# Kernel tuning notes

Hardware: AMD Instinct MI355X
Metric: run time of the kernel (lower is better)

Reference implementation:

```python
import jax, jax.numpy as jnp
import numpy as np

DIM = 180
WS = 16        # window_size
OWS = 24       # overlap_win_size = int(16*0.5)+16
HEADS = 6
HD = DIM // HEADS
MLP_HID = DIM * 2
TABLE = (WS + OWS - 1) ** 2  # 1521
H = W = 256
B = 1


def layernorm(x, g, b, eps=1e-5):
    mu = x.mean(-1, keepdims=True)
    d = x - mu
    var = (d * d).mean(-1, keepdims=True)
    return g * d / jnp.sqrt(var + eps) + b


def setup_inputs() -> dict:
    key = jax.random.key(0)
    ks = jax.random.split(key, 12)
    std = 0.02
    inp = {
        'x': jax.random.normal(ks[0], (B, H * W, DIM), jnp.float32),
        'rpi': jax.random.randint(ks[1], (WS * WS, OWS * OWS), 0, TABLE, jnp.int32),
        'h': H,
        'w': W,
        'norm1_g': jnp.ones((DIM,), jnp.float32),
        'norm1_b': jnp.zeros((DIM,), jnp.float32),
        'q_w': jax.random.normal(ks[2], (DIM, DIM), jnp.float32) * std,
        'q_b': jnp.zeros((DIM,), jnp.float32),
        'kv_w': jax.random.normal(ks[3], (DIM, 2 * DIM), jnp.float32) * std,
        'kv_b': jnp.zeros((2 * DIM,), jnp.float32),
        'rpb_table': jax.random.normal(ks[4], (TABLE, HEADS), jnp.float32) * std,
        'proj_w': jax.random.normal(ks[5], (DIM, DIM), jnp.float32) * std,
        'proj_b': jnp.zeros((DIM,), jnp.float32),
        'norm2_g': jnp.ones((DIM,), jnp.float32),
        'norm2_b': jnp.zeros((DIM,), jnp.float32),
        'mlp_w1': jax.random.normal(ks[6], (DIM, MLP_HID), jnp.float32) * std,
        'mlp_b1': jnp.zeros((MLP_HID,), jnp.float32),
        'mlp_w2': jax.random.normal(ks[7], (MLP_HID, DIM), jnp.float32) * std,
        'mlp_b2': jnp.zeros((DIM,), jnp.float32),
    }
    return inp


def reference(x, rpi, h, w, norm1_g, norm1_b, q_w, q_b, kv_w, kv_b,
              rpb_table, proj_w, proj_b, norm2_g, norm2_b,
              mlp_w1, mlp_b1, mlp_w2, mlp_b2):
    b, L, c = x.shape
    ws, ows, heads = WS, OWS, HEADS
    d = c // heads
    scale = d ** -0.5
    pad = (ows - ws) // 2  # 4
    nh, nw = h // ws, w // ws
    nq, n = ws * ws, ows * ows
    b_ = b * nh * nw

    shortcut = x
    xn = layernorm(x, norm1_g, norm1_b)
    x_img = xn.reshape(b, h, w, c)

    q = x_img @ q_w + q_b                    # [b,h,w,c]
    kv = x_img @ kv_w + kv_b                 # [b,h,w,2c] (k | v)

    # window_partition for q -> [b_, nq, c]
    qw = q.reshape(b, nh, ws, nw, ws, c).transpose(0, 1, 3, 2, 4, 5)
    qw = qw.reshape(b_, nq, c)

    # nn.Unfold(kernel=ows, stride=ws, padding=pad) on kv -> overlapping windows
    kvp = jnp.pad(kv, ((0, 0), (pad, pad), (pad, pad), (0, 0)))
    rows = (jnp.arange(nh) * ws)[:, None] + jnp.arange(ows)   # [nh, ows]
    cols = (jnp.arange(nw) * ws)[:, None] + jnp.arange(ows)   # [nw, ows]
    t = kvp[:, rows]                         # [b, nh, ows, W+2p, 2c]
    t = t[:, :, :, cols]                     # [b, nh, ows, nw, ows, 2c]
    t = t.transpose(0, 1, 3, 2, 4, 5).reshape(b_, n, 2 * c)
    k_win, v_win = t[..., :c], t[..., c:]

    qh = qw.reshape(b_, nq, heads, d).transpose(0, 2, 1, 3) * scale
    kh = k_win.reshape(b_, n, heads, d).transpose(0, 2, 1, 3)
    vh = v_win.reshape(b_, n, heads, d).transpose(0, 2, 1, 3)

    attn = jnp.einsum('bhqd,bhkd->bhqk', qh, kh)              # [b_,heads,nq,n]
    bias = rpb_table[rpi.reshape(-1)].reshape(nq, n, heads).transpose(2, 0, 1)
    attn = jax.nn.softmax(attn + bias[None], axis=-1)
    out = jnp.einsum('bhqk,bhkd->bhqd', attn, vh)
    out = out.transpose(0, 2, 1, 3).reshape(b_, nq, c)

    # window_reverse -> [b, h*w, c]
    xo = out.reshape(b, nh, nw, ws, ws, c).transpose(0, 1, 3, 2, 4, 5)
    xo = xo.reshape(b, h * w, c)

    xo = xo @ proj_w + proj_b + shortcut
    xn2 = layernorm(xo, norm2_g, norm2_b)
    mlp = jax.nn.gelu(xn2 @ mlp_w1 + mlp_b1, approximate=False) @ mlp_w2 + mlp_b2
    return xo + mlp
```

## Files before the change

kernel.cpp:

```cpp
#include <hip/hip_runtime.h>
#include <hip/hip_bf16.h>
#include <stdint.h>

#define DIM 180
#define WS 16
#define OWS 24
#define HEADS 6
#define HD 30
#define MLP_HID 360
#define HH 256
#define WW 256
#define L (HH * WW)
#define NWIN 256
#define NQ 256
#define NK 576

#define KP1 192
#define KP2 384
#define NQKV 576

#define QSCALE 0.2633988734672831f
#define LOG2E 1.4426950408889634f

typedef float f4v __attribute__((ext_vector_type(4)));
typedef short s8v __attribute__((ext_vector_type(8)));
typedef short s4v __attribute__((ext_vector_type(4)));

static __device__ __forceinline__ short f2bf(float x) {
    union { __hip_bfloat16 h; short s; } u;
    u.h = __float2bfloat16(x);
    return u.s;
}
static __device__ __forceinline__ uint32_t pack_bf2(float lo, float hi) {
    union { __hip_bfloat162 h; uint32_t u; } u;
    u.h.x = __float2bfloat16(lo);
    u.h.y = __float2bfloat16(hi);
    return u.u;
}

typedef __attribute__((address_space(1))) const unsigned int ga_u32;
typedef __attribute__((address_space(3))) unsigned int la_u32;
static __device__ __forceinline__ void gld16(const void* g, void* l) {
    __builtin_amdgcn_global_load_lds((ga_u32*)g, (la_u32*)l, 16, 0, 0);
}

__global__ __launch_bounds__(64) void ln_kernel(const float* __restrict__ x,
                                                const float* __restrict__ g,
                                                const float* __restrict__ b,
                                                __hip_bfloat16* __restrict__ out) {
    int row = blockIdx.x;
    int t = threadIdx.x;
    const float* xr = x + (size_t)row * DIM;
    float v0 = xr[t];
    float v1 = xr[t + 64];
    float v2 = (t < DIM - 128) ? xr[t + 128] : 0.f;
    float s = v0 + v1 + v2;
    #pragma unroll
    for (int o = 32; o > 0; o >>= 1) s += __shfl_down(s, o);
    s = __shfl(s, 0);
    float mu = s * (1.f / DIM);
    float d0 = v0 - mu, d1 = v1 - mu;
    float d2 = (t < DIM - 128) ? (v2 - mu) : 0.f;
    float vs = d0 * d0 + d1 * d1 + d2 * d2;
    #pragma unroll
    for (int o = 32; o > 0; o >>= 1) vs += __shfl_down(vs, o);
    vs = __shfl(vs, 0);
    float rstd = rsqrtf(vs * (1.f / DIM) + 1e-5f);
    __hip_bfloat16* orow = out + (size_t)row * KP1;
    orow[t]      = __float2bfloat16(g[t] * d0 * rstd + b[t]);
    orow[t + 64] = __float2bfloat16(g[t + 64] * d1 * rstd + b[t + 64]);
    if (t < DIM - 128)
        orow[t + 128] = __float2bfloat16(g[t + 128] * d2 * rstd + b[t + 128]);
    if (t < KP1 - DIM) orow[DIM + t] = __float2bfloat16(0.f);
}

__global__ __launch_bounds__(256) void bias_kernel(const int* __restrict__ rpi,
                                                   const float* __restrict__ rpb,
                                                   float* __restrict__ biasC) {
    int idx = blockIdx.x * 256 + threadIdx.x;
    int j = idx & 15;
    int q = (idx >> 4) & 255;
    int r = idx >> 12;
    int kc = r % 36;
    int head = r / 36;
    int k = kc * 16 + j;
    int t = rpi[q * NK + k];
    biasC[idx] = rpb[t * HEADS + head] * LOG2E;
}

__global__ __launch_bounds__(256) void wconv_kernel(
        const float* __restrict__ qw, const float* __restrict__ kvw,
        const float* __restrict__ pw, const float* __restrict__ w1,
        const float* __restrict__ w2, short* __restrict__ wt) {
    int idx = blockIdx.x * 256 + threadIdx.x;
    float v = 0.f;
    if (idx < 110592) {
        int n = idx / KP1, k = idx - n * KP1;
        if (k < DIM) {
            if (n < DIM) v = qw[k * DIM + n] * QSCALE;
            else if (n < 540) v = kvw[k * (2 * DIM) + (n - DIM)];
        }
    } else if (idx < 147456) {
        int r = idx - 110592;
        int n = r / KP1, k = r - n * KP1;
        if (k < DIM && n < DIM) v = pw[k * DIM + n];
    } else if (idx < 221184) {
        int r = idx - 147456;
        int n = r / KP1, k = r - n * KP1;
        if (k < DIM && n < MLP_HID) v = w1[k * MLP_HID + n];
    } else {
        int r = idx - 221184;
        int n = r / KP2, k = r - n * KP2;
        if (k < MLP_HID && n < DIM) v = w2[k * DIM + n];
    }
    wt[idx] = f2bf(v);
}

__global__ __launch_bounds__(256) void bconv_kernel(
        const float* __restrict__ qb, const float* __restrict__ kvb,
        const float* __restrict__ pb, const float* __restrict__ b1,
        const float* __restrict__ b2, float* __restrict__ bv) {
    int idx = blockIdx.x * 256 + threadIdx.x;
    if (idx >= 1344) return;
    float v = 0.f;
    if (idx < 576) {
        if (idx < DIM) v = qb[idx] * QSCALE;
        else if (idx < 540) v = kvb[idx - DIM];
    } else if (idx < 768) {
        int n = idx - 576; if (n < DIM) v = pb[n];
    } else if (idx < 1152) {
        int n = idx - 768; if (n < MLP_HID) v = b1[n];
    } else {
        int n = idx - 1152; if (n < DIM) v = b2[n];
    }
    bv[idx] = v;
}

__global__ __launch_bounds__(256) void mgemm(
        const short* __restrict__ A, const short* __restrict__ Wt,
        const float* __restrict__ bias,
        float* __restrict__ outf, short* __restrict__ outb,
        int lda, int ldo, int nK, int mode) {
    __shared__ short As[2][128 * 32];
    __shared__ short Wsm[2][64 * 32];
    int tid = threadIdx.x;
    int lane = tid & 63, wave = tid >> 6;
    int q15 = lane & 15, quad = lane >> 4;
    int n0 = blockIdx.x * 64;
    int m0 = blockIdx.y * 128;

    auto stage = [&](int buf, int k0) {
        int lr = lane >> 2, c = lane & 3;
        const short* Ab = A + (size_t)m0 * lda + k0;
        #pragma unroll
        for (int i = 0; i < 2; i++) {
            int r = i * 64 + wave * 16 + lr;
            gld16(Ab + (size_t)r * lda + ((c ^ (r & 3)) * 8),
                  &As[buf][(i * 64 + wave * 16) * 32]);
        }
        const short* Wb = Wt + (size_t)n0 * lda + k0;
        {
            int r = wave * 16 + lr;
            gld16(Wb + (size_t)r * lda + ((c ^ (r & 3)) * 8),
                  &Wsm[buf][(wave * 16) * 32]);
        }
    };

    f4v acc[2][4];
    #pragma unroll
    for (int a = 0; a < 2; a++)
        #pragma unroll
        for (int b = 0; b < 4; b++) acc[a][b] = (f4v){0.f, 0.f, 0.f, 0.f};

    stage(0, 0);
    __syncthreads();
    for (int ch = 0; ch < nK; ch++) {
        int buf = ch & 1;
        if (ch + 1 < nK) stage(buf ^ 1, (ch + 1) * 32);
        s8v af[2], wf[4];
        #pragma unroll
        for (int mt = 0; mt < 2; mt++) {
            int r = wave * 32 + mt * 16 + q15;
            af[mt] = *(const s8v*)&As[buf][r * 32 + ((quad ^ (r & 3)) * 8)];
        }
        #pragma unroll
        for (int nt = 0; nt < 4; nt++) {
            int r = nt * 16 + q15;
            wf[nt] = *(const s8v*)&Wsm[buf][r * 32 + ((quad ^ (r & 3)) * 8)];
        }
        #pragma unroll
        for (int mt = 0; mt < 2; mt++)
            #pragma unroll
            for (int nt = 0; nt < 4; nt++)
                acc[mt][nt] = __builtin_amdgcn_mfma_f32_16x16x32_bf16(
                    af[mt], wf[nt], acc[mt][nt], 0, 0, 0);
        __syncthreads();
    }

    #pragma unroll
    for (int mt = 0; mt < 2; mt++) {
        int mb = m0 + wave * 32 + mt * 16 + quad * 4;
        #pragma unroll
        for (int nt = 0; nt < 4; nt++) {
            int n = n0 + nt * 16 + q15;
            float bv = bias[n];
            f4v a = acc[mt][nt];
            #pragma unroll
            for (int r = 0; r < 4; r++) {
                int m = mb + r;
                float v = a[r] + bv;
                if (mode == 0) {
                    outb[(size_t)m * ldo + n] = f2bf(v);
                } else if (mode == 1) {
                    float ge = 0.5f * v * (1.f + erff(v * 0.70710678118654752f));
                    outb[(size_t)m * ldo + n] = f2bf(ge);
                } else {
                    if (n < DIM) outf[(size_t)m * DIM + n] += v;
                }
            }
        }
    }
}

__global__ __launch_bounds__(256) void projln(
        const short* __restrict__ A, const short* __restrict__ Wt,
        const float* __restrict__ bias, const float* __restrict__ resid,
        const float* __restrict__ g2, const float* __restrict__ b2,
        float* __restrict__ outf, short* __restrict__ outb) {
    __shared__ short As[2][64 * 32];
    __shared__ short Wsm[2][192 * 32];
    int tid = threadIdx.x;
    int lane = tid & 63, wave = tid >> 6;
    int q15 = lane & 15, quad = lane >> 4;
    int m0 = blockIdx.x * 64;

    auto stage = [&](int buf, int k0) {
        int lr = lane >> 2, c = lane & 3;
        const short* Ab = A + (size_t)m0 * KP1 + k0;
        {
            int r = wave * 16 + lr;
            gld16(Ab + (size_t)r * KP1 + ((c ^ (r & 3)) * 8),
                  &As[buf][(wave * 16) * 32]);
        }
        #pragma unroll
        for (int i = 0; i < 3; i++) {
            int r = i * 64 + wave * 16 + lr;
            gld16(Wt + (size_t)r * KP1 + k0 + ((c ^ (r & 3)) * 8),
                  &Wsm[buf][(i * 64 + wave * 16) * 32]);
        }
    };

    f4v acc[12];
    #pragma unroll
    for (int b = 0; b < 12; b++) acc[b] = (f4v){0.f, 0.f, 0.f, 0.f};

    stage(0, 0);
    __syncthreads();
    for (int ch = 0; ch < KP1 / 32; ch++) {
        int buf = ch & 1;
        if (ch + 1 < KP1 / 32) stage(buf ^ 1, (ch + 1) * 32);
        int ra = wave * 16 + q15;
        s8v af = *(const s8v*)&As[buf][ra * 32 + ((quad ^ (ra & 3)) * 8)];
        #pragma unroll
        for (int nt = 0; nt < 12; nt++) {
            int r = nt * 16 + q15;
            s8v wf = *(const s8v*)&Wsm[buf][r * 32 + ((quad ^ (r & 3)) * 8)];
            acc[nt] = __builtin_amdgcn_mfma_f32_16x16x32_bf16(af, wf, acc[nt], 0, 0, 0);
        }
        __syncthreads();
    }

    float gv[12], bv[12], biasv[12];
    #pragma unroll
    for (int nt = 0; nt < 12; nt++) {
        int n = nt * 16 + q15;
        biasv[nt] = bias[n];
        gv[nt] = (n < DIM) ? g2[n] : 0.f;
        bv[nt] = (n < DIM) ? b2[n] : 0.f;
    }
    int mb = m0 + wave * 16 + quad * 4;
    #pragma unroll
    for (int r = 0; r < 4; r++) {
        int m = mb + r;
        float v[12];
        float s = 0.f, ss = 0.f;
        #pragma unroll
        for (int nt = 0; nt < 12; nt++) {
            int n = nt * 16 + q15;
            float x = acc[nt][r] + biasv[nt];
            if (n < DIM) x += resid[(size_t)m * DIM + n];
            else x = 0.f;
            v[nt] = x;
            s += x;
            ss += x * x;
        }
        #pragma unroll
        for (int o = 8; o > 0; o >>= 1) {
            s += __shfl_xor(s, o);
            ss += __shfl_xor(ss, o);
        }
        float mu = s * (1.f / DIM);
        float var = ss * (1.f / DIM) - mu * mu;
        float rstd = rsqrtf(var + 1e-5f);
        #pragma unroll
        for (int nt = 0; nt < 12; nt++) {
            int n = nt * 16 + q15;
            if (n < DIM) outf[(size_t)m * DIM + n] = v[nt];
            outb[(size_t)m * KP1 + n] = f2bf(gv[nt] * (v[nt] - mu) * rstd + bv[nt]);
        }
    }
}

#define CHUNK 32
#define NCHUNK (NK / CHUNK)

__global__ __launch_bounds__(256) void attn_kernel(
        const __hip_bfloat16* __restrict__ qkvb,
        const float* __restrict__ biasC, __hip_bfloat16* __restrict__ aout) {
    __shared__ __align__(16) short Ks[2][CHUNK][32];
    __shared__ __align__(16) short Vt[2][32][40];
    __shared__ __align__(16) short Ps[256][40];

    int tid = threadIdx.x;
    int lane = tid & 63;
    int wave = tid >> 6;
    int q15 = lane & 15;
    int quad = lane >> 4;
    int head = blockIdx.x % HEADS;
    int win = blockIdx.x / HEADS;
    int bh = win >> 4, bw = win & 15;

    const uint32_t* kvd = (const uint32_t*)qkvb;

    s8v qf[4];
    #pragma unroll
    for (int qt = 0; qt < 4; qt++) {
        int q = wave * 64 + qt * 16 + q15;
        int qy = q >> 4, qx = q & 15;
        size_t pos = (size_t)(bh * WS + qy) * WW + (bw * WS + qx);
        const uint32_t* qp = kvd + pos * 288 + head * 15 + quad * 4;
        uint32_t w0 = qp[0], w1 = qp[1], w2 = qp[2], w3 = qp[3];
        union { uint32_t u[4]; s8v v; } cv;
        cv.u[0] = w0; cv.u[1] = w1; cv.u[2] = w2; cv.u[3] = w3;
        qf[qt] = cv.v;
    }
    if (head == 0) {
        int qy = tid >> 4, qx = tid & 15;
        size_t pos = (size_t)(bh * WS + qy) * WW + (bw * WS + qx);
        uint2 z = make_uint2(0u, 0u);
        uint2* oz = (uint2*)(aout + pos * KP1 + DIM);
        oz[0] = z; oz[1] = z; oz[2] = z;
    }

    uint32_t ka, kb, va, vb;
    int keyK = tid >> 3, pK = tid & 7;
    int keyV = tid & 31, pp = tid >> 5;

    auto rowbase = [&](int jk) -> const uint32_t* {
        int oy = jk / OWS, ox = jk - oy * OWS;
        int y = bh * WS - 4 + oy, x = bw * WS - 4 + ox;
        if ((unsigned)y < HH && (unsigned)x < WW)
            return kvd + ((size_t)y * WW + x) * 288;
        return nullptr;
    };
    auto loadKV = [&](int c0) {
        ka = kb = va = vb = 0u;
        const uint32_t* rk = rowbase(c0 + keyK);
        if (rk) {
            const uint32_t* kp = rk + 90 + head * 15 + pK * 2;
            ka = kp[0];
            if (pK < 7) kb = kp[1];
        }
        const uint32_t* rv = rowbase(c0 + keyV);
        if (rv) {
            const uint32_t* vp = rv + 180 + head * 15 + pp * 2;
            va = vp[0];
            if (pp < 7) vb = vp[1];
        }
    };
    auto writeKV = [&](int bufi) {
        *(uint2*)&Ks[bufi][keyK][pK * 4] = make_uint2(ka, kb);
        int d0 = pp * 4;
        Vt[bufi][d0][keyV]     = (short)(va & 0xffff);
        Vt[bufi][d0 + 1][keyV] = (short)(va >> 16);
        if (pp < 7) {
            Vt[bufi][d0 + 2][keyV] = (short)(vb & 0xffff);
            Vt[bufi][d0 + 3][keyV] = (short)(vb >> 16);
        } else {
            Vt[bufi][30][keyV] = (short)0x3F80;
            Vt[bufi][31][keyV] = 0;
        }
    };

    loadKV(0);
    writeKV(0);
    __syncthreads();

    f4v oacc[2][4];
    #pragma unroll
    for (int a = 0; a < 2; a++)
        #pragma unroll
        for (int b = 0; b < 4; b++) oacc[a][b] = (f4v){0.f, 0.f, 0.f, 0.f};

    const float* bC = biasC + (size_t)head * (36 * 256 * 16);

    for (int ch = 0; ch < NCHUNK; ch++) {
        int buf = ch & 1;
        if (ch + 1 < NCHUNK) loadKV((ch + 1) * CHUNK);

        s8v kf[2];
        #pragma unroll
        for (int kt = 0; kt < 2; kt++)
            kf[kt] = *(const s8v*)&Ks[buf][kt * 16 + q15][quad * 8];
        #pragma unroll
        for (int qt = 0; qt < 4; qt++) {
            int q = wave * 64 + qt * 16 + q15;
            #pragma unroll
            for (int kt = 0; kt < 2; kt++) {
                int kc = ch * 2 + kt;
                f4v c = *(const f4v*)(bC + ((size_t)kc * 256 + q) * 16 + quad * 4);
                c = __builtin_amdgcn_mfma_f32_16x16x32_bf16(kf[kt], qf[qt], c, 0, 0, 0);
                s4v pk;
                #pragma unroll
                for (int r = 0; r < 4; r++)
                    pk[r] = f2bf(__builtin_amdgcn_exp2f(c[r]));
                *(s4v*)&Ps[q][kt * 16 + quad * 4] = pk;
            }
        }

        s8v va0 = *(const s8v*)&Vt[buf][q15][quad * 8];
        s8v va1 = *(const s8v*)&Vt[buf][16 + q15][quad * 8];
        #pragma unroll
        for (int nt = 0; nt < 4; nt++) {
            s8v pb = *(const s8v*)&Ps[wave * 64 + nt * 16 + q15][quad * 8];
            oacc[0][nt] = __builtin_amdgcn_mfma_f32_16x16x32_bf16(va0, pb, oacc[0][nt], 0, 0, 0);
            oacc[1][nt] = __builtin_amdgcn_mfma_f32_16x16x32_bf16(va1, pb, oacc[1][nt], 0, 0, 0);
        }

        if (ch + 1 < NCHUNK) writeKV(buf ^ 1);
        __syncthreads();
    }

    #pragma unroll
    for (int nt = 0; nt < 4; nt++) {
        float l = __shfl(oacc[1][nt][2], 48 | q15);
        float rl = 1.0f / l;
        int q = wave * 64 + nt * 16 + q15;
        int qy = q >> 4, qx = q & 15;
        size_t pos = (size_t)(bh * WS + qy) * WW + (bw * WS + qx);
        uint32_t* od = (uint32_t*)(aout + pos * KP1 + head * HD);
        int dh = quad * 2;
        f4v o0 = oacc[0][nt], o1 = oacc[1][nt];
        od[dh]     = pack_bf2(o0[0] * rl, o0[1] * rl);
        od[dh + 1] = pack_bf2(o0[2] * rl, o0[3] * rl);
        od[8 + dh] = pack_bf2(o1[0] * rl, o1[1] * rl);
        if (quad < 3)
            od[8 + dh + 1] = pack_bf2(o1[2] * rl, o1[3] * rl);
    }
}

extern "C" void kernel_launch(void* const* d_in, const int* in_sizes, int n_in,
                              void* d_out, int out_size, void* d_ws, size_t ws_size,
                              hipStream_t stream) {
    const float* x      = (const float*)d_in[0];
    const int*   rpi    = (const int*)d_in[1];
    const float* n1g    = (const float*)d_in[4];
    const float* n1b    = (const float*)d_in[5];
    const float* q_w    = (const float*)d_in[6];
    const float* q_b    = (const float*)d_in[7];
    const float* kv_w   = (const float*)d_in[8];
    const float* kv_b   = (const float*)d_in[9];
    const float* rpb    = (const float*)d_in[10];
    const float* proj_w = (const float*)d_in[11];
    const float* proj_b = (const float*)d_in[12];
    const float* n2g    = (const float*)d_in[13];
    const float* n2b    = (const float*)d_in[14];
    const float* w1     = (const float*)d_in[15];
    const float* b1     = (const float*)d_in[16];
    const float* w2     = (const float*)d_in[17];
    const float* b2     = (const float*)d_in[18];
    float* out = (float*)d_out;

    char* ws = (char*)d_ws;
    short* qkvb  = (short*)(ws);
    short* xn    = (short*)(ws + 75497472ull);
    float* biasC = (float*)(ws + 100663296ull);
    short* wt    = (short*)(ws + 104202240ull);
    short* wt_qkv  = wt;
    short* wt_proj = wt + 110592;
    short* wt_1    = wt + 147456;
    short* wt_2    = wt + 221184;
    float* bvec  = (float*)(ws + 104202240ull + 589824ull);
    float* b_qkv  = bvec;
    float* b_proj = bvec + 576;
    float* b_1    = bvec + 768;
    float* b_2    = bvec + 1152;
    short* ao  = xn;
    short* xn2 = qkvb;
    short* h1  = qkvb + 12582912;

    bias_kernel<<<884736 / 256, 256, 0, stream>>>(rpi, rpb, biasC);
    wconv_kernel<<<294912 / 256, 256, 0, stream>>>(q_w, kv_w, proj_w, w1, w2, wt);
    bconv_kernel<<<6, 256, 0, stream>>>(q_b, kv_b, proj_b, b1, b2, bvec);
    ln_kernel<<<L, 64, 0, stream>>>(x, n1g, n1b, (__hip_bfloat16*)xn);
    mgemm<<<dim3(NQKV / 64, L / 128), 256, 0, stream>>>(
        xn, wt_qkv, b_qkv, nullptr, qkvb, KP1, NQKV, KP1 / 32, 0);
    attn_kernel<<<NWIN * HEADS, 256, 0, stream>>>(
        (const __hip_bfloat16*)qkvb, biasC, (__hip_bfloat16*)ao);
    projln<<<L / 64, 256, 0, stream>>>(
        ao, wt_proj, b_proj, x, n2g, n2b, out, xn2);
    mgemm<<<dim3(KP2 / 64, L / 128), 256, 0, stream>>>(
        xn2, wt_1, b_1, nullptr, h1, KP1, KP2, KP1 / 32, 1);
    mgemm<<<dim3(KP1 / 64, L / 128), 256, 0, stream>>>(
        h1, wt_2, b_2, out, nullptr, KP2, 0, KP2 / 32, 3);
}
```

Before: 422.3 us.

## Keep softmax probabilities in registers by permuting key order across MFMAs

The attention kernel no longer stages exp'd scores through a shared-memory P buffer. It permutes which key rows feed each QK MFMA, and reorders the precomputed bias layout to match, so that the QK output fragment lines up directly with the B-operand layout of the PV MFMA. The probabilities are packed in registers and fed straight into the PV MFMA. This removes LDS writes and reads plus their bank traffic and frees LDS for occupancy, but it depends on the key permutation being consistent between bias, K rows and V rows.

After: 435.8 us. +3.2%, slower.

```diff
diff --git a/kernel.cpp b/kernel.cpp
--- a/kernel.cpp
+++ b/kernel.cpp
@@ -83,7 +83,7 @@
     int r = idx >> 12;
     int kc = r % 36;
     int head = r / 36;
-    int k = kc * 16 + j;
+    int k = (kc >> 1) * 32 + ((j >> 2) << 3) + ((kc & 1) << 2) + (j & 3);
     int t = rpi[q * NK + k];
     biasC[idx] = rpb[t * HEADS + head] * LOG2E;
 }
@@ -319,7 +319,6 @@
         const float* __restrict__ biasC, __hip_bfloat16* __restrict__ aout) {
     __shared__ __align__(16) short Ks[2][CHUNK][32];
     __shared__ __align__(16) short Vt[2][32][40];
-    __shared__ __align__(16) short Ps[256][40];
 
     int tid = threadIdx.x;
     int lane = tid & 63;
@@ -403,38 +402,32 @@
         for (int b = 0; b < 4; b++) oacc[a][b] = (f4v){0.f, 0.f, 0.f, 0.f};
 
     const float* bC = biasC + (size_t)head * (36 * 256 * 16);
+    int pr = ((q15 & 12) << 1) | (q15 & 3);
 
     for (int ch = 0; ch < NCHUNK; ch++) {
         int buf = ch & 1;
         if (ch + 1 < NCHUNK) loadKV((ch + 1) * CHUNK);
 
-        s8v kf[2];
-        #pragma unroll
-        for (int kt = 0; kt < 2; kt++)
-            kf[kt] = *(const s8v*)&Ks[buf][kt * 16 + q15][quad * 8];
+        s8v kf0 = *(const s8v*)&Ks[buf][pr][quad * 8];
+        s8v kf1 = *(const s8v*)&Ks[buf][pr + 4][quad * 8];
+        s8v va0 = *(const s8v*)&Vt[buf][q15][quad * 8];
+        s8v va1 = *(const s8v*)&Vt[buf][16 + q15][quad * 8];
+
+        const float* bc0 = bC + ((size_t)(ch * 2) * 256) * 16 + quad * 4;
         #pragma unroll
         for (int qt = 0; qt < 4; qt++) {
             int q = wave * 64 + qt * 16 + q15;
-            #pragma unroll
-            for (int kt = 0; kt < 2; kt++) {
-                int kc = ch * 2 + kt;
-                f4v c = *(const f4v*)(bC + ((size_t)kc * 256 + q) * 16 + quad * 4);
-                c = __builtin_amdgcn_mfma_f32_16x16x32_bf16(kf[kt], qf[qt], c, 0, 0, 0);
-                s4v pk;
-                #pragma unroll
-                for (int r = 0; r < 4; r++)
-                    pk[r] = f2bf(__builtin_amdgcn_exp2f(c[r]));
-                *(s4v*)&Ps[q][kt * 16 + quad * 4] = pk;
-            }
-        }
-
-        s8v va0 = *(const s8v*)&Vt[buf][q15][quad * 8];
-        s8v va1 = *(const s8v*)&Vt[buf][16 + q15][quad * 8];
-        #pragma unroll
-        for (int nt = 0; nt < 4; nt++) {
-            s8v pb = *(const s8v*)&Ps[wave * 64 + nt * 16 + q15][quad * 8];
-            oacc[0][nt] = __builtin_amdgcn_mfma_f32_16x16x32_bf16(va0, pb, oacc[0][nt], 0, 0, 0);
-            oacc[1][nt] = __builtin_amdgcn_mfma_f32_16x16x32_bf16(va1, pb, oacc[1][nt], 0, 0, 0);
+            f4v c0 = *(const f4v*)(bc0 + (size_t)q * 16);
+            f4v c1 = *(const f4v*)(bc0 + 256 * 16 + (size_t)q * 16);
+            c0 = __builtin_amdgcn_mfma_f32_16x16x32_bf16(kf0, qf[qt], c0, 0, 0, 0);
+            c1 = __builtin_amdgcn_mfma_f32_16x16x32_bf16(kf1, qf[qt], c1, 0, 0, 0);
+            union { uint32_t u[4]; s8v v; } pbv;
+            pbv.u[0] = pack_bf2(__builtin_amdgcn_exp2f(c0[0]), __builtin_amdgcn_exp2f(c0[1]));
+            pbv.u[1] = pack_bf2(__builtin_amdgcn_exp2f(c0[2]), __builtin_amdgcn_exp2f(c0[3]));
+            pbv.u[2] = pack_bf2(__builtin_amdgcn_exp2f(c1[0]), __builtin_amdgcn_exp2f(c1[1]));
+            pbv.u[3] = pack_bf2(__builtin_amdgcn_exp2f(c1[2]), __builtin_amdgcn_exp2f(c1[3]));
+            oacc[0][qt] = __builtin_amdgcn_mfma_f32_16x16x32_bf16(va0, pbv.v, oacc[0][qt], 0, 0, 0);
+            oacc[1][qt] = __builtin_amdgcn_mfma_f32_16x16x32_bf16(va1, pbv.v, oacc[1][qt], 0, 0, 0);
         }
 
         if (ch + 1 < NCHUNK) writeKV(buf ^ 1);
```

## Keep attention probabilities in registers and deepen KV/bias prefetch pipeline

Applied to the files above, without the earlier changes.

Removes the shared-memory P staging buffer by permuting K rows so the QK^T MFMA output layout directly matches the B-operand layout of the PV MFMA, packing exp2 results into registers. The bias table is reordered to match this permuted key order. KV global loads are now prefetched two chunks ahead using alternating register sets, and bias for the next chunk is loaded early into the accumulator registers. This cuts LDS traffic and hides global latency, at the cost of higher register pressure.

After: 418.6 us. Within noise of the previous version (-0.9%).

```diff
diff --git a/kernel.cpp b/kernel.cpp
--- a/kernel.cpp
+++ b/kernel.cpp
@@ -83,7 +83,7 @@
     int r = idx >> 12;
     int kc = r % 36;
     int head = r / 36;
-    int k = kc * 16 + j;
+    int k = (kc >> 1) * 32 + ((j >> 2) << 3) + ((kc & 1) << 2) + (j & 3);
     int t = rpi[q * NK + k];
     biasC[idx] = rpb[t * HEADS + head] * LOG2E;
 }
@@ -319,7 +319,6 @@
         const float* __restrict__ biasC, __hip_bfloat16* __restrict__ aout) {
     __shared__ __align__(16) short Ks[2][CHUNK][32];
     __shared__ __align__(16) short Vt[2][32][40];
-    __shared__ __align__(16) short Ps[256][40];
 
     int tid = threadIdx.x;
     int lane = tid & 63;
@@ -352,7 +351,6 @@
         oz[0] = z; oz[1] = z; oz[2] = z;
     }
 
-    uint32_t ka, kb, va, vb;
     int keyK = tid >> 3, pK = tid & 7;
     int keyV = tid & 31, pp = tid >> 5;
 
@@ -363,7 +361,7 @@
             return kvd + ((size_t)y * WW + x) * 288;
         return nullptr;
     };
-    auto loadKV = [&](int c0) {
+    auto loadKV = [&](int c0, uint32_t& ka, uint32_t& kb, uint32_t& va, uint32_t& vb) {
         ka = kb = va = vb = 0u;
         const uint32_t* rk = rowbase(c0 + keyK);
         if (rk) {
@@ -378,7 +376,7 @@
             if (pp < 7) vb = vp[1];
         }
     };
-    auto writeKV = [&](int bufi) {
+    auto writeKV = [&](int bufi, uint32_t ka, uint32_t kb, uint32_t va, uint32_t vb) {
         *(uint2*)&Ks[bufi][keyK][pK * 4] = make_uint2(ka, kb);
         int d0 = pp * 4;
         Vt[bufi][d0][keyV]     = (short)(va & 0xffff);
@@ -392,8 +390,24 @@
         }
     };
 
-    loadKV(0);
-    writeKV(0);
+    const float* bC  = biasC + (size_t)head * (36 * 256 * 16);
+    const float* bCl = bC + ((size_t)(wave * 64 + q15)) * 16 + quad * 4;
+    f4v cb[2][4];
+    auto loadBias = [&](int ch) {
+        #pragma unroll
+        for (int kt = 0; kt < 2; kt++)
+            #pragma unroll
+            for (int qt = 0; qt < 4; qt++)
+                cb[kt][qt] = *(const f4v*)(bCl + ((size_t)(ch * 2 + kt) * 256 + qt * 16) * 16);
+    };
+
+    uint32_t kaA, kbA, vaA, vbA;
+    uint32_t kaB, kbB, vaB, vbB;
+
+    loadKV(0,     kaA, kbA, vaA, vbA);
+    loadKV(CHUNK, kaB, kbB, vaB, vbB);
+    loadBias(0);
+    writeKV(0, kaA, kbA, vaA, vbA);
     __syncthreads();
 
     f4v oacc[2][4];
@@ -402,43 +416,49 @@
         #pragma unroll
         for (int b = 0; b < 4; b++) oacc[a][b] = (f4v){0.f, 0.f, 0.f, 0.f};
 
-    const float* bC = biasC + (size_t)head * (36 * 256 * 16);
-
-    for (int ch = 0; ch < NCHUNK; ch++) {
-        int buf = ch & 1;
-        if (ch + 1 < NCHUNK) loadKV((ch + 1) * CHUNK);
-
-        s8v kf[2];
-        #pragma unroll
-        for (int kt = 0; kt < 2; kt++)
-            kf[kt] = *(const s8v*)&Ks[buf][kt * 16 + q15][quad * 8];
+    int pr = ((q15 & 12) << 1) | (q15 & 3);
+
+    auto body = [&](int ch, int bufR,
+                    uint32_t& kaR, uint32_t& kbR, uint32_t& vaR, uint32_t& vbR,
+                    uint32_t& kaW, uint32_t& kbW, uint32_t& vaW, uint32_t& vbW) {
+        s8v kf0 = *(const s8v*)&Ks[bufR][pr][quad * 8];
+        s8v kf1 = *(const s8v*)&Ks[bufR][pr + 4][quad * 8];
+        s8v va0 = *(const s8v*)&Vt[bufR][q15][quad * 8];
+        s8v va1 = *(const s8v*)&Vt[bufR][16 + q15][quad * 8];
+
         #pragma unroll
         for (int qt = 0; qt < 4; qt++) {
-            int q = wave * 64 + qt * 16 + q15;
-            #pragma unroll
-            for (int kt = 0; kt < 2; kt++) {
-                int kc = ch * 2 + kt;
-                f4v c = *(const f4v*)(bC + ((size_t)kc * 256 + q) * 16 + quad * 4);
-                c = __builtin_amdgcn_mfma_f32_16x16x32_bf16(kf[kt], qf[qt], c, 0, 0, 0);
-                s4v pk;
-                #pragma unroll
-                for (int r = 0; r < 4; r++)
-                    pk[r] = f2bf(__builtin_amdgcn_exp2f(c[r]));
-                *(s4v*)&Ps[q][kt * 16 + quad * 4] = pk;
-            }
-        }
-
-        s8v va0 = *(const s8v*)&Vt[buf][q15][quad * 8];
-        s8v va1 = *(const s8v*)&Vt[buf][16 + q15][quad * 8];
-        #pragma unroll
-        for (int nt = 0; nt < 4; nt++) {
-            s8v pb = *(const s8v*)&Ps[wave * 64 + nt * 16 + q15][quad * 8];
-            oacc[0][nt] = __builtin_amdgcn_mfma_f32_16x16x32_bf16(va0, pb, oacc[0][nt], 0, 0, 0);
-            oacc[1][nt] = __builtin_amdgcn_mfma_f32_16x16x32_bf16(va1, pb, oacc[1][nt], 0, 0, 0);
-        }
-
-        if (ch + 1 < NCHUNK) writeKV(buf ^ 1);
+            cb[0][qt] = __builtin_amdgcn_mfma_f32_16x16x32_bf16(kf0, qf[qt], cb[0][qt], 0, 0, 0);
+            cb[1][qt] = __builtin_amdgcn_mfma_f32_16x16x32_bf16(kf1, qf[qt], cb[1][qt], 0, 0, 0);
+        }
+        if (ch + 2 < NCHUNK) loadKV((ch + 2) * CHUNK, kaR, kbR, vaR, vbR);
+
+        s8v pbv[4];
+        #pragma unroll
+        for (int qt = 0; qt < 4; qt++) {
+            union { uint32_t u[4]; s8v v; } pk;
+            pk.u[0] = pack_bf2(__builtin_amdgcn_exp2f(cb[0][qt][0]), __builtin_amdgcn_exp2f(cb[0][qt][1]));
+            pk.u[1] = pack_bf2(__builtin_amdgcn_exp2f(cb[0][qt][2]), __builtin_amdgcn_exp2f(cb[0][qt][3]));
+            pk.u[2] = pack_bf2(__builtin_amdgcn_exp2f(cb[1][qt][0]), __builtin_amdgcn_exp2f(cb[1][qt][1]));
+            pk.u[3] = pack_bf2(__builtin_amdgcn_exp2f(cb[1][qt][2]), __builtin_amdgcn_exp2f(cb[1][qt][3]));
+            pbv[qt] = pk.v;
+        }
+        if (ch + 1 < NCHUNK) loadBias(ch + 1);
+
+        #pragma unroll
+        for (int qt = 0; qt < 4; qt++) {
+            oacc[0][qt] = __builtin_amdgcn_mfma_f32_16x16x32_bf16(va0, pbv[qt], oacc[0][qt], 0, 0, 0);
+            oacc[1][qt] = __builtin_amdgcn_mfma_f32_16x16x32_bf16(va1, pbv[qt], oacc[1][qt], 0, 0, 0);
+        }
+
+        if (ch + 1 < NCHUNK) writeKV(bufR ^ 1, kaW, kbW, vaW, vbW);
         __syncthreads();
+    };
+
+    #pragma unroll 1
+    for (int t = 0; t < NCHUNK / 2; t++) {
+        body(2 * t,     0, kaA, kbA, vaA, vbA, kaB, kbB, vaB, vbB);
+        body(2 * t + 1, 1, kaB, kbB, vaB, vbB, kaA, kbA, vaA, vbA);
     }
 
     #pragma unroll
```
